# Kernel tuning notes

Hardware: AMD Instinct MI355X
Metric: run time of the kernel (lower is better)

The kernel has to match this reference:

```python
import jax, jax.numpy as jnp
import numpy as np

B, TQ, TK = 2, 2048, 2048
H, E, D = 16, 256, 4096       # num_heads, embed_dim, d_model
DH = D // H                   # head_dim == embed_dim (required by per-head RMSNorm(embed_dim))
LAMBDA_INIT = 0.8
LAYER_INDEX = 0
EPS = 1.1920929e-07           # torch RMSNorm default eps = finfo(float32).eps


def setup_inputs() -> dict:
    key = jax.random.key(0)
    ks = jax.random.split(key, 14)
    s = 0.02
    lam_init_val = LAMBDA_INIT - 0.6 * float(np.exp(-0.3 * LAYER_INDEX))
    return {
        "x": jax.random.normal(ks[0], (B, TQ, E), jnp.float32),
        "encoder_out": jax.random.normal(ks[1], (B, TK, E), jnp.float32),
        "Wq": jax.random.normal(ks[2], (H, E, DH), jnp.float32) * s,
        "bq": jnp.zeros((H, DH), jnp.float32),
        "Wk": jax.random.normal(ks[3], (H, E, DH), jnp.float32) * s,
        "bk": jnp.zeros((H, DH), jnp.float32),
        "Wv": jax.random.normal(ks[4], (H, E, DH), jnp.float32) * s,
        "bv": jnp.zeros((H, DH), jnp.float32),
        "lq1": jax.random.normal(ks[5], (H, DH), jnp.float32) * 0.1,
        "lk1": jax.random.normal(ks[6], (H, DH), jnp.float32) * 0.1,
        "lq2": jax.random.normal(ks[7], (H, DH), jnp.float32) * 0.1,
        "lk2": jax.random.normal(ks[8], (H, DH), jnp.float32) * 0.1,
        "lam_init": jnp.full((H,), lam_init_val, jnp.float32),
        "g": jnp.ones((H, DH), jnp.float32),     # per-head RMSNorm weight
        "Wo": jax.random.normal(ks[9], (D, E), jnp.float32) * s,
        "bo": jnp.zeros((E,), jnp.float32),
    }


def reference(x, encoder_out, Wq, bq, Wk, bk, Wv, bv,
              lq1, lk1, lq2, lk2, lam_init, g, Wo, bo):
    # per-head projections, vectorized over heads: [B,H,T,DH]
    q = jnp.einsum('bte,hed->bhtd', x, Wq) + bq[:, None, :]
    k = jnp.einsum('bse,hed->bhsd', encoder_out, Wk) + bk[:, None, :]
    v = jnp.einsum('bse,hed->bhsd', encoder_out, Wv) + bv[:, None, :]
    dh2 = DH // 2
    q1, q2 = q[..., :dh2], q[..., dh2:]
    k1, k2 = k[..., :dh2], k[..., dh2:]
    scale = 1.0 / jnp.sqrt(jnp.float32(dh2))
    s1 = jax.nn.softmax(jnp.einsum('bhtd,bhsd->bhts', q1, k1) * scale, axis=-1)
    s2 = jax.nn.softmax(jnp.einsum('bhtd,bhsd->bhts', q2, k2) * scale, axis=-1)
    # learned per-head lambda scalar
    lam = jnp.exp(jnp.sum(lq1 * lk1, axis=-1)) - jnp.exp(jnp.sum(lq2 * lk2, axis=-1)) + lam_init  # [H]
    w = s1 - lam[None, :, None, None] * s2
    o = jnp.einsum('bhts,bhsd->bhtd', w, v)
    # per-head RMSNorm + (1 - lambda_init) scaling
    rms = jnp.sqrt(jnp.mean(o * o, axis=-1, keepdims=True) + EPS)
    o = (1.0 - LAMBDA_INIT) * (o / rms) * g[None, :, None, :]
    # concat heads -> output projection
    o = o.transpose(0, 2, 1, 3).reshape(B, TQ, D)
    return o @ Wo + bo
```

## Files before the change

### kernel.cpp

```cpp
#include <hip/hip_runtime.h>
#include <hip/hip_bf16.h>
#include <stdint.h>
#include <math.h>

typedef __bf16 bf16;
typedef __bf16 bf16x8 __attribute__((ext_vector_type(8)));
typedef float f32x4 __attribute__((ext_vector_type(4)));
typedef unsigned int u32;

#define MFMA16(a, b, c) __builtin_amdgcn_mfma_f32_16x16x32_bf16(a, b, c, 0, 0, 0)

typedef const u32 __attribute__((address_space(1)))* gptr1;
typedef u32 __attribute__((address_space(3)))* lptr3;

__device__ __forceinline__ void load_lds16(const void* g, void* l) {
    __builtin_amdgcn_global_load_lds((gptr1)g, (lptr3)l, 16, 0, 0);
}

#define SCALE_QK 0.08838834764831845f
#define LOG2E 1.4426950408889634f
#define QK_PRESCALE (SCALE_QK * LOG2E)
#define RMS_EPS 1.1920929e-07f
#define OUT_SCALE 0.2f
#define DEFER_THR 8.0f

__global__ void cvt_act(const float* __restrict__ x, const float* __restrict__ enc,
                        bf16* __restrict__ xb, bf16* __restrict__ eb) {
    int gid = blockIdx.x * 256 + threadIdx.x;
    const float* src = (gid < 131072) ? x : enc;
    bf16* dst = (gid < 131072) ? xb : eb;
    int i = (gid & 131071) * 8;
    float4 v0 = *(const float4*)(src + i);
    float4 v1 = *(const float4*)(src + i + 4);
    union { bf16 h[8]; uint4 u; } p;
    p.h[0] = (bf16)v0.x; p.h[1] = (bf16)v0.y; p.h[2] = (bf16)v0.z; p.h[3] = (bf16)v0.w;
    p.h[4] = (bf16)v1.x; p.h[5] = (bf16)v1.y; p.h[6] = (bf16)v1.z; p.h[7] = (bf16)v1.w;
    *(uint4*)(dst + i) = p.u;
}

__global__ void txp_w(const float* __restrict__ Wq, const float* __restrict__ Wk,
                      const float* __restrict__ Wv,
                      bf16* __restrict__ WTq, bf16* __restrict__ WTk, bf16* __restrict__ WTv) {
    int z = blockIdx.z; int iw = z >> 4, hh = z & 15;
    const float* src = (iw == 0 ? Wq : iw == 1 ? Wk : Wv) + hh * 65536;
    bf16* dst = (iw == 0 ? WTq : iw == 1 ? WTk : WTv) + hh * 65536;
    __shared__ bf16 T[64][68];
    int r0 = blockIdx.y * 64, c0 = blockIdx.x * 64;
    int tid = threadIdx.x;
#pragma unroll
    for (int t = 0; t < 4; ++t) {
        int idx = tid + t * 256;
        int row = idx >> 4, c4 = (idx & 15) * 4;
        float4 v = *(const float4*)(src + (r0 + row) * 256 + c0 + c4);
        T[row][c4] = (bf16)v.x; T[row][c4 + 1] = (bf16)v.y;
        T[row][c4 + 2] = (bf16)v.z; T[row][c4 + 3] = (bf16)v.w;
    }
    __syncthreads();
#pragma unroll
    for (int t = 0; t < 2; ++t) {
        int idx = tid + t * 256;
        int crow = idx >> 3, r8 = (idx & 7) * 8;
        union { bf16 h[8]; uint4 u; } p;
#pragma unroll
        for (int j = 0; j < 8; ++j) p.h[j] = T[r8 + j][crow];
        *(uint4*)(dst + (c0 + crow) * 256 + r0 + r8) = p.u;
    }
}

__global__ void txp_wo(const float* __restrict__ Wo, bf16* __restrict__ WoT) {
    __shared__ bf16 T[64][68];
    int r0 = blockIdx.y * 64, c0 = blockIdx.x * 64;
    int tid = threadIdx.x;
#pragma unroll
    for (int t = 0; t < 4; ++t) {
        int idx = tid + t * 256;
        int row = idx >> 4, c4 = (idx & 15) * 4;
        float4 v = *(const float4*)(Wo + (size_t)(r0 + row) * 256 + c0 + c4);
        T[row][c4] = (bf16)v.x; T[row][c4 + 1] = (bf16)v.y;
        T[row][c4 + 2] = (bf16)v.z; T[row][c4 + 3] = (bf16)v.w;
    }
    __syncthreads();
#pragma unroll
    for (int t = 0; t < 2; ++t) {
        int idx = tid + t * 256;
        int crow = idx >> 3, r8 = (idx & 7) * 8;
        union { bf16 h[8]; uint4 u; } p;
#pragma unroll
        for (int j = 0; j < 8; ++j) p.h[j] = T[r8 + j][crow];
        *(uint4*)(WoT + (size_t)(c0 + crow) * 4096 + r0 + r8) = p.u;
    }
}

__global__ void txp_v(const bf16* __restrict__ V, bf16* __restrict__ VT) {
    int bh = blockIdx.z;
    const bf16* src = V + (size_t)bh * 2048 * 256;
    bf16* dst = VT + (size_t)bh * 256 * 2048;
    __shared__ bf16 T[64][68];
    int s0 = blockIdx.x * 64, d0 = blockIdx.y * 64;
    int tid = threadIdx.x;
#pragma unroll
    for (int t = 0; t < 2; ++t) {
        int idx = tid + t * 256;
        int row = idx >> 3, c8 = (idx & 7) * 8;
        uint4 v = *(const uint4*)(src + (s0 + row) * 256 + d0 + c8);
        *(uint2*)&T[row][c8] = make_uint2(v.x, v.y);
        *(uint2*)&T[row][c8 + 4] = make_uint2(v.z, v.w);
    }
    __syncthreads();
#pragma unroll
    for (int t = 0; t < 2; ++t) {
        int idx = tid + t * 256;
        int crow = idx >> 3, r8 = (idx & 7) * 8;
        union { bf16 h[8]; uint4 u; } p;
#pragma unroll
        for (int j = 0; j < 8; ++j) p.h[j] = T[r8 + j][crow];
        *(uint4*)(dst + (d0 + crow) * 2048 + s0 + r8) = p.u;
    }
}

__global__ void lam_kernel(const float* __restrict__ lq1, const float* __restrict__ lk1,
                           const float* __restrict__ lq2, const float* __restrict__ lk2,
                           const float* __restrict__ lam_init, float* __restrict__ lam_out) {
    int tid = threadIdx.x; int hh = tid >> 4, i = tid & 15;
    float s1 = 0.f, s2 = 0.f;
#pragma unroll
    for (int j = 0; j < 16; ++j) {
        int d = i + j * 16;
        s1 += lq1[hh * 256 + d] * lk1[hh * 256 + d];
        s2 += lq2[hh * 256 + d] * lk2[hh * 256 + d];
    }
#pragma unroll
    for (int msk = 1; msk < 16; msk <<= 1) { s1 += __shfl_xor(s1, msk); s2 += __shfl_xor(s2, msk); }
    if (i == 0) lam_out[hh] = __expf(s1) - __expf(s2) + lam_init[hh];
}

__global__ __launch_bounds__(256) void proj_gemm(
    const bf16* __restrict__ xb, const bf16* __restrict__ eb,
    const bf16* __restrict__ WTq, const bf16* __restrict__ WTk, const bf16* __restrict__ WTv,
    const float* __restrict__ bq, const float* __restrict__ bk, const float* __restrict__ bv,
    bf16* __restrict__ Qb, bf16* __restrict__ Kb, bf16* __restrict__ Vb) {
    int z = blockIdx.z;
    const bf16* A = (z == 0) ? xb : eb;
    const bf16* BT = (z == 0) ? WTq : (z == 1) ? WTk : WTv;
    const float* bias = (z == 0) ? bq : (z == 1) ? bk : bv;
    bf16* out = (z == 0) ? Qb : (z == 1) ? Kb : Vb;
    float qs = (z == 0) ? QK_PRESCALE : 1.0f;

    __shared__ alignas(16) bf16 As[128 * 32];
    __shared__ alignas(16) bf16 Bs[128 * 32];
    int m0 = blockIdx.x * 128, n0 = blockIdx.y * 128;
    int tid = threadIdx.x, w = tid >> 6, lane = tid & 63;
    int lrow = lane & 15, lgrp = lane >> 4, lk8 = lgrp * 8;
    int wr = (w >> 1) * 64, wc = (w & 1) * 64;

    f32x4 acc[4][4];
#pragma unroll
    for (int i = 0; i < 4; ++i)
#pragma unroll
        for (int j = 0; j < 4; ++j) acc[i][j] = (f32x4){0.f, 0.f, 0.f, 0.f};

    for (int k0 = 0; k0 < 256; k0 += 32) {
        __syncthreads();
#pragma unroll
        for (int t = 0; t < 2; ++t) {
            int c = tid + t * 256;
            int row = c >> 2, k8 = (c & 3) * 8;
            load_lds16(A + (m0 + row) * 256 + k0 + k8, &As[c * 8]);
            load_lds16(BT + (n0 + row) * 256 + k0 + k8, &Bs[c * 8]);
        }
        __syncthreads();
        bf16x8 af[4], bfr[4];
#pragma unroll
        for (int f = 0; f < 4; ++f) af[f] = *(const bf16x8*)&As[(wr + f * 16 + lrow) * 32 + lk8];
#pragma unroll
        for (int f = 0; f < 4; ++f) bfr[f] = *(const bf16x8*)&Bs[(wc + f * 16 + lrow) * 32 + lk8];
#pragma unroll
        for (int i = 0; i < 4; ++i)
#pragma unroll
            for (int j = 0; j < 4; ++j) acc[i][j] = MFMA16(af[i], bfr[j], acc[i][j]);
    }
#pragma unroll
    for (int i = 0; i < 4; ++i) {
#pragma unroll
        for (int j = 0; j < 4; ++j) {
            int n = n0 + wc + j * 16 + lrow;
            float bvv = bias[n];
            int hh = n >> 8, d = n & 255;
#pragma unroll
            for (int r = 0; r < 4; ++r) {
                int m = m0 + wr + i * 16 + lgrp * 4 + r;
                int bb = m >> 11, tt = m & 2047;
                out[(((size_t)bb * 16 + hh) * 2048 + tt) * 256 + d] = (bf16)((acc[i][j][r] + bvv) * qs);
            }
        }
    }
}

__global__ __launch_bounds__(256, 2) void attn_kernel(
    const bf16* __restrict__ Qb, const bf16* __restrict__ Kb, const bf16* __restrict__ VTb,
    const float* __restrict__ lam_ws, const float* __restrict__ g, bf16* __restrict__ On) {
    __shared__ alignas(16) bf16 Ks[2][32 * 256];
    __shared__ alignas(16) bf16 VTs[2][256 * 32];
    __shared__ alignas(16) bf16 Ps[4][16 * 72];

    int orig = blockIdx.x;
    int xcd = orig & 7, idx = orig >> 3;
    int bh = xcd * 4 + (idx >> 5);
    int qb = idx & 31;
    int b = bh >> 4, h = bh & 15;
    int q0 = qb * 64;

    int tid = threadIdx.x, w = tid >> 6, lane = tid & 63;
    int lrow = lane & 15, lgrp = lane >> 4, lk8 = lgrp * 8;
    int ksw = lrow & 7;
    int vsw = (lrow >> 1) & 3;

    const bf16* Qg = Qb + ((size_t)bh * 2048 + q0 + w * 16) * 256;
    bf16x8 qf[8];
#pragma unroll
    for (int kk = 0; kk < 8; ++kk)
        qf[kk] = *(const bf16x8*)(Qg + lrow * 256 + kk * 32 + lk8);

    f32x4 o1[16], o2[16];
#pragma unroll
    for (int i = 0; i < 16; ++i) { o1[i] = (f32x4){0.f,0.f,0.f,0.f}; o2[i] = (f32x4){0.f,0.f,0.f,0.f}; }
    float m1[4], l1[4], m2[4], l2[4];
#pragma unroll
    for (int r = 0; r < 4; ++r) { m1[r] = -1e30f; l1[r] = 0.f; m2[r] = -1e30f; l2[r] = 0.f; }

    const bf16* Kg = Kb + (size_t)bh * 2048 * 256;
    const bf16* VTg = VTb + (size_t)bh * 256 * 2048;
    bf16* Pw = &Ps[w][0];

    auto STAGE = [&](int buf, int kt) {
        int s0 = kt * 32;
#pragma unroll
        for (int i = 0; i < 4; ++i) {
            int s = i * 256 + tid;
            int row = s >> 5;
            int cg = (s & 31) ^ (row & 7);
            load_lds16(Kg + (size_t)(s0 + row) * 256 + cg * 8, &Ks[buf][s * 8]);
        }
#pragma unroll
        for (int i = 0; i < 4; ++i) {
            int s = i * 256 + tid;
            int row = s >> 2;
            int cg = (s & 3) ^ ((row >> 1) & 3);
            load_lds16(VTg + (size_t)row * 2048 + s0 + cg * 8, &VTs[buf][s * 8]);
        }
    };

    STAGE(0, 0);
    __syncthreads();

    int cur = 0;
    for (int kt = 0; kt < 64; ++kt) {
        if (kt + 1 < 64) STAGE(cur ^ 1, kt + 1);

        const bf16* Kbuf = &Ks[cur][0];
        const bf16* Vbuf = &VTs[cur][0];

        f32x4 s1a = (f32x4){0.f,0.f,0.f,0.f}, s1b = s1a, s2a = s1a, s2b = s1a;
        __builtin_amdgcn_s_setprio(1);
#pragma unroll
        for (int kk = 0; kk < 4; ++kk) {
            int c1 = (kk * 4 + lgrp) ^ ksw;
            int c2 = (16 + kk * 4 + lgrp) ^ ksw;
            bf16x8 k1a = *(const bf16x8*)&Kbuf[lrow * 256 + (c1 << 3)];
            bf16x8 k1b = *(const bf16x8*)&Kbuf[(16 + lrow) * 256 + (c1 << 3)];
            bf16x8 k2a = *(const bf16x8*)&Kbuf[lrow * 256 + (c2 << 3)];
            bf16x8 k2b = *(const bf16x8*)&Kbuf[(16 + lrow) * 256 + (c2 << 3)];
            s1a = MFMA16(qf[kk], k1a, s1a);
            s1b = MFMA16(qf[kk], k1b, s1b);
            s2a = MFMA16(qf[4 + kk], k2a, s2a);
            s2b = MFMA16(qf[4 + kk], k2b, s2b);
        }
        __builtin_amdgcn_s_setprio(0);

        float lmx1 = fmaxf(fmaxf(s1a[0], s1b[0]), fmaxf(s1a[1], s1b[1]));
        lmx1 = fmaxf(lmx1, fmaxf(fmaxf(s1a[2], s1b[2]), fmaxf(s1a[3], s1b[3])));
        float lmx2 = fmaxf(fmaxf(s2a[0], s2b[0]), fmaxf(s2a[1], s2b[1]));
        lmx2 = fmaxf(lmx2, fmaxf(fmaxf(s2a[2], s2b[2]), fmaxf(s2a[3], s2b[3])));
        float mmin1 = fminf(fminf(m1[0], m1[1]), fminf(m1[2], m1[3]));
        float mmin2 = fminf(fminf(m2[0], m2[1]), fminf(m2[2], m2[3]));

        if (!__all((lmx1 <= mmin1 + DEFER_THR) ? 1 : 0)) {
            float mt[4];
#pragma unroll
            for (int r = 0; r < 4; ++r) mt[r] = fmaxf(s1a[r], s1b[r]);
#pragma unroll
            for (int msk = 1; msk < 16; msk <<= 1)
#pragma unroll
                for (int r = 0; r < 4; ++r) mt[r] = fmaxf(mt[r], __shfl_xor(mt[r], msk));
            float c[4];
#pragma unroll
            for (int r = 0; r < 4; ++r) {
                float mn = fmaxf(m1[r], mt[r]);
                c[r] = exp2f(m1[r] - mn);
                m1[r] = mn; l1[r] *= c[r];
            }
#pragma unroll
            for (int df = 0; df < 16; ++df)
#pragma unroll
                for (int r = 0; r < 4; ++r) o1[df][r] *= c[r];
        }
        if (!__all((lmx2 <= mmin2 + DEFER_THR) ? 1 : 0)) {
            float mt[4];
#pragma unroll
            for (int r = 0; r < 4; ++r) mt[r] = fmaxf(s2a[r], s2b[r]);
#pragma unroll
            for (int msk = 1; msk < 16; msk <<= 1)
#pragma unroll
                for (int r = 0; r < 4; ++r) mt[r] = fmaxf(mt[r], __shfl_xor(mt[r], msk));
            float c[4];
#pragma unroll
            for (int r = 0; r < 4; ++r) {
                float mn = fmaxf(m2[r], mt[r]);
                c[r] = exp2f(m2[r] - mn);
                m2[r] = mn; l2[r] *= c[r];
            }
#pragma unroll
            for (int df = 0; df < 16; ++df)
#pragma unroll
                for (int r = 0; r < 4; ++r) o2[df][r] *= c[r];
        }
#pragma unroll
        for (int r = 0; r < 4; ++r) {
            float p10 = exp2f(s1a[r] - m1[r]);
            float p11 = exp2f(s1b[r] - m1[r]);
            float p20 = exp2f(s2a[r] - m2[r]);
            float p21 = exp2f(s2b[r] - m2[r]);
            l1[r] += p10 + p11;
            l2[r] += p20 + p21;
            int prow = (lgrp * 4 + r) * 72;
            Pw[prow + lrow] = (bf16)p10;
            Pw[prow + 16 + lrow] = (bf16)p11;
            Pw[prow + 32 + lrow] = (bf16)p20;
            Pw[prow + 48 + lrow] = (bf16)p21;
        }

        bf16x8 pa1 = *(const bf16x8*)&Pw[lrow * 72 + lk8];
        bf16x8 pa2 = *(const bf16x8*)&Pw[lrow * 72 + 32 + lk8];
        __builtin_amdgcn_s_setprio(1);
#pragma unroll
        for (int df = 0; df < 16; ++df) {
            int vc = lgrp ^ vsw;
            bf16x8 vb = *(const bf16x8*)&Vbuf[(df * 16 + lrow) * 32 + (vc << 3)];
            o1[df] = MFMA16(pa1, vb, o1[df]);
            o2[df] = MFMA16(pa2, vb, o2[df]);
        }
        __builtin_amdgcn_s_setprio(0);

        __syncthreads();
        cur ^= 1;
    }

#pragma unroll
    for (int msk = 1; msk < 16; msk <<= 1)
#pragma unroll
        for (int r = 0; r < 4; ++r) {
            l1[r] += __shfl_xor(l1[r], msk);
            l2[r] += __shfl_xor(l2[r], msk);
        }
    float lam = lam_ws[h];
    float i1[4], i2[4], ssq[4];
#pragma unroll
    for (int r = 0; r < 4; ++r) { i1[r] = 1.f / l1[r]; i2[r] = lam / l2[r]; ssq[r] = 0.f; }
#pragma unroll
    for (int df = 0; df < 16; ++df)
#pragma unroll
        for (int r = 0; r < 4; ++r) {
            float v = o1[df][r] * i1[r] - o2[df][r] * i2[r];
            o1[df][r] = v;
            ssq[r] += v * v;
        }
#pragma unroll
    for (int msk = 1; msk < 16; msk <<= 1)
#pragma unroll
        for (int r = 0; r < 4; ++r) ssq[r] += __shfl_xor(ssq[r], msk);
    float rinv[4];
#pragma unroll
    for (int r = 0; r < 4; ++r) rinv[r] = 1.f / sqrtf(ssq[r] * (1.f / 256.f) + RMS_EPS);
#pragma unroll
    for (int df = 0; df < 16; ++df) {
        int d = df * 16 + lrow;
        float gv = g[h * 256 + d] * OUT_SCALE;
#pragma unroll
        for (int r = 0; r < 4; ++r) {
            int t = q0 + w * 16 + lgrp * 4 + r;
            On[((size_t)b * 2048 + t) * 4096 + h * 256 + d] = (bf16)(o1[df][r] * rinv[r] * gv);
        }
    }
}

__global__ __launch_bounds__(256) void out_gemm(const bf16* __restrict__ A, const bf16* __restrict__ BT,
                                                const float* __restrict__ bo, float* __restrict__ out) {
    __shared__ alignas(16) bf16 As[64 * 32];
    __shared__ alignas(16) bf16 Bs[64 * 32];
    int m0 = blockIdx.x * 64, n0 = blockIdx.y * 64;
    int tid = threadIdx.x, w = tid >> 6, lane = tid & 63;
    int lrow = lane & 15, lgrp = lane >> 4, lk8 = lgrp * 8;
    int wr = (w >> 1) * 32, wc = (w & 1) * 32;
    f32x4 acc[2][2];
#pragma unroll
    for (int i = 0; i < 2; ++i)
#pragma unroll
        for (int j = 0; j < 2; ++j) acc[i][j] = (f32x4){0.f, 0.f, 0.f, 0.f};
    for (int k0 = 0; k0 < 4096; k0 += 32) {
        __syncthreads();
        int row = tid >> 2, k8 = (tid & 3) * 8;
        load_lds16(A + (size_t)(m0 + row) * 4096 + k0 + k8, &As[tid * 8]);
        load_lds16(BT + (size_t)(n0 + row) * 4096 + k0 + k8, &Bs[tid * 8]);
        __syncthreads();
        bf16x8 af[2], bfr[2];
#pragma unroll
        for (int f = 0; f < 2; ++f) {
            af[f] = *(const bf16x8*)&As[(wr + f * 16 + lrow) * 32 + lk8];
            bfr[f] = *(const bf16x8*)&Bs[(wc + f * 16 + lrow) * 32 + lk8];
        }
#pragma unroll
        for (int i = 0; i < 2; ++i)
#pragma unroll
            for (int j = 0; j < 2; ++j) acc[i][j] = MFMA16(af[i], bfr[j], acc[i][j]);
    }
#pragma unroll
    for (int i = 0; i < 2; ++i)
#pragma unroll
        for (int j = 0; j < 2; ++j) {
            int n = n0 + wc + j * 16 + lrow;
            float bv = bo[n];
#pragma unroll
            for (int r = 0; r < 4; ++r) {
                int m = m0 + wr + i * 16 + lgrp * 4 + r;
                out[(size_t)m * 256 + n] = acc[i][j][r] + bv;
            }
        }
}

extern "C" void kernel_launch(void* const* d_in, const int* in_sizes, int n_in,
                              void* d_out, int out_size, void* d_ws, size_t ws_size,
                              hipStream_t stream) {
    const float* x = (const float*)d_in[0];
    const float* enc = (const float*)d_in[1];
    const float* Wq = (const float*)d_in[2];
    const float* bq = (const float*)d_in[3];
    const float* Wk = (const float*)d_in[4];
    const float* bk = (const float*)d_in[5];
    const float* Wv = (const float*)d_in[6];
    const float* bv = (const float*)d_in[7];
    const float* lq1 = (const float*)d_in[8];
    const float* lk1 = (const float*)d_in[9];
    const float* lq2 = (const float*)d_in[10];
    const float* lk2 = (const float*)d_in[11];
    const float* lam_init = (const float*)d_in[12];
    const float* g = (const float*)d_in[13];
    const float* Wo = (const float*)d_in[14];
    const float* bo = (const float*)d_in[15];
    float* out = (float*)d_out;

    char* ws = (char*)d_ws;
    const size_t MB = 1024 * 1024;
    bf16* xb  = (bf16*)(ws + 0 * MB);
    bf16* eb  = (bf16*)(ws + 2 * MB);
    bf16* WTq = (bf16*)(ws + 4 * MB);
    bf16* WTk = (bf16*)(ws + 6 * MB);
    bf16* WTv = (bf16*)(ws + 8 * MB);
    bf16* WoT = (bf16*)(ws + 10 * MB);
    float* lam = (float*)(ws + 12 * MB);
    bf16* Qb  = (bf16*)(ws + 13 * MB);
    bf16* Kb  = (bf16*)(ws + 45 * MB);
    bf16* Vb  = (bf16*)(ws + 77 * MB);
    bf16* VTb = (bf16*)(ws + 109 * MB);
    bf16* On  = Vb;

    hipLaunchKernelGGL(cvt_act, dim3(1024), dim3(256), 0, stream, x, enc, xb, eb);
    hipLaunchKernelGGL(txp_w, dim3(4, 4, 48), dim3(256), 0, stream, Wq, Wk, Wv, WTq, WTk, WTv);
    hipLaunchKernelGGL(txp_wo, dim3(4, 64, 1), dim3(256), 0, stream, Wo, WoT);
    hipLaunchKernelGGL(lam_kernel, dim3(1), dim3(256), 0, stream, lq1, lk1, lq2, lk2, lam_init, lam);
    hipLaunchKernelGGL(proj_gemm, dim3(32, 32, 3), dim3(256), 0, stream,
                       xb, eb, WTq, WTk, WTv, bq, bk, bv, Qb, Kb, Vb);
    hipLaunchKernelGGL(txp_v, dim3(32, 4, 32), dim3(256), 0, stream, Vb, VTb);
    hipLaunchKernelGGL(attn_kernel, dim3(1024), dim3(256), 0, stream, Qb, Kb, VTb, lam, g, On);
    hipLaunchKernelGGL(out_gemm, dim3(64, 4), dim3(256), 0, stream, On, WoT, bo, out);
}
```

Baseline: 385.8 us.

## Switch attention to 32x32 MFMA with per-wave softmax branch split

Rewrites the attention kernel so each wave owns one of the two differential softmax branches for 32 query rows and uses 32x32x16 MFMA. The score tile is computed transposed (K as A operand), and probabilities are repacked into the PV operand with cross-half lane shuffles instead of a round trip through shared memory. Per-row rescale factors are exchanged through LDS, and the two branches are combined at the end through a shared-memory buffer before the RMSNorm. The aim is higher MFMA efficiency, fewer LDS P writes and fewer registers per wave. The cost is extra LDS traffic and barriers in the epilogue, plus a larger shared-memory footprint that may limit occupancy.

```diff
diff --git a/kernel.cpp b/kernel.cpp
--- a/kernel.cpp
+++ b/kernel.cpp
@@ -6,15 +6,26 @@
 typedef __bf16 bf16;
 typedef __bf16 bf16x8 __attribute__((ext_vector_type(8)));
 typedef float f32x4 __attribute__((ext_vector_type(4)));
+typedef float f32x16 __attribute__((ext_vector_type(16)));
 typedef unsigned int u32;
 
 #define MFMA16(a, b, c) __builtin_amdgcn_mfma_f32_16x16x32_bf16(a, b, c, 0, 0, 0)
+#define MFMA32(a, b, c) __builtin_amdgcn_mfma_f32_32x32x16_bf16(a, b, c, 0, 0, 0)
 
 typedef const u32 __attribute__((address_space(1)))* gptr1;
 typedef u32 __attribute__((address_space(3)))* lptr3;
 
 __device__ __forceinline__ void load_lds16(const void* g, void* l) {
     __builtin_amdgcn_global_load_lds((gptr1)g, (lptr3)l, 16, 0, 0);
+}
+
+__device__ __forceinline__ u32 pk2(float lo, float hi_) {
+    union { bf16 h[2]; u32 u; } t;
+    t.h[0] = (bf16)lo; t.h[1] = (bf16)hi_;
+    return t.u;
+}
+__device__ __forceinline__ u32 xswap(u32 x) {
+    return (u32)__shfl_xor((int)x, 32);
 }
 
 #define SCALE_QK 0.08838834764831845f
@@ -199,9 +210,14 @@
 __global__ __launch_bounds__(256, 2) void attn_kernel(
     const bf16* __restrict__ Qb, const bf16* __restrict__ Kb, const bf16* __restrict__ VTb,
     const float* __restrict__ lam_ws, const float* __restrict__ g, bf16* __restrict__ On) {
-    __shared__ alignas(16) bf16 Ks[2][32 * 256];
-    __shared__ alignas(16) bf16 VTs[2][256 * 32];
-    __shared__ alignas(16) bf16 Ps[4][16 * 72];
+    __shared__ alignas(16) char SMEM[75264];
+    bf16* KsB = (bf16*)SMEM;
+    bf16* VsB = (bf16*)(SMEM + 32768);
+    float* o2buf  = (float*)SMEM;
+    float* smem_c = (float*)(SMEM + 65536);
+    float* smem_i = (float*)(SMEM + 66048);
+    float* smem_r = (float*)(SMEM + 66560);
+    float* psum   = (float*)(SMEM + 66816);
 
     int orig = blockIdx.x;
     int xcd = orig & 7, idx = orig >> 3;
@@ -211,26 +227,27 @@
     int q0 = qb * 64;
 
     int tid = threadIdx.x, w = tid >> 6, lane = tid & 63;
-    int lrow = lane & 15, lgrp = lane >> 4, lk8 = lgrp * 8;
-    int ksw = lrow & 7;
-    int vsw = (lrow >> 1) & 3;
-
-    const bf16* Qg = Qb + ((size_t)bh * 2048 + q0 + w * 16) * 256;
+    int lq = lane & 31, hi = lane >> 5;
+    int br = w >> 1, qw = (w & 1) * 32;
+    int ksw = lq & 7;
+    int vsw = (lq >> 1) & 3;
+    bool hib = (hi != 0);
+
+    const bf16* Qg = Qb + ((size_t)bh * 2048 + q0 + qw + lq) * 256 + br * 128;
     bf16x8 qf[8];
 #pragma unroll
-    for (int kk = 0; kk < 8; ++kk)
-        qf[kk] = *(const bf16x8*)(Qg + lrow * 256 + kk * 32 + lk8);
-
-    f32x4 o1[16], o2[16];
-#pragma unroll
-    for (int i = 0; i < 16; ++i) { o1[i] = (f32x4){0.f,0.f,0.f,0.f}; o2[i] = (f32x4){0.f,0.f,0.f,0.f}; }
-    float m1[4], l1[4], m2[4], l2[4];
-#pragma unroll
-    for (int r = 0; r < 4; ++r) { m1[r] = -1e30f; l1[r] = 0.f; m2[r] = -1e30f; l2[r] = 0.f; }
+    for (int dk = 0; dk < 8; ++dk)
+        qf[dk] = *(const bf16x8*)(Qg + dk * 16 + hi * 8);
+
+    f32x16 o[8];
+#pragma unroll
+    for (int dt = 0; dt < 8; ++dt)
+#pragma unroll
+        for (int i = 0; i < 16; ++i) o[dt][i] = 0.f;
+    float m = -1e30f, lsum = 0.f;
 
     const bf16* Kg = Kb + (size_t)bh * 2048 * 256;
     const bf16* VTg = VTb + (size_t)bh * 256 * 2048;
-    bf16* Pw = &Ps[w][0];
 
     auto STAGE = [&](int buf, int kt) {
         int s0 = kt * 32;
@@ -239,14 +256,14 @@
             int s = i * 256 + tid;
             int row = s >> 5;
             int cg = (s & 31) ^ (row & 7);
-            load_lds16(Kg + (size_t)(s0 + row) * 256 + cg * 8, &Ks[buf][s * 8]);
+            load_lds16(Kg + (size_t)(s0 + row) * 256 + cg * 8, KsB + buf * 8192 + s * 8);
         }
 #pragma unroll
         for (int i = 0; i < 4; ++i) {
             int s = i * 256 + tid;
             int row = s >> 2;
             int cg = (s & 3) ^ ((row >> 1) & 3);
-            load_lds16(VTg + (size_t)row * 2048 + s0 + cg * 8, &VTs[buf][s * 8]);
+            load_lds16(VTg + (size_t)row * 2048 + s0 + cg * 8, VsB + buf * 8192 + s * 8);
         }
     };
 
@@ -256,98 +273,77 @@
     int cur = 0;
     for (int kt = 0; kt < 64; ++kt) {
         if (kt + 1 < 64) STAGE(cur ^ 1, kt + 1);
-
-        const bf16* Kbuf = &Ks[cur][0];
-        const bf16* Vbuf = &VTs[cur][0];
-
-        f32x4 s1a = (f32x4){0.f,0.f,0.f,0.f}, s1b = s1a, s2a = s1a, s2b = s1a;
+        const bf16* Kbuf = KsB + cur * 8192;
+        const bf16* Vbuf = VsB + cur * 8192;
+
+        f32x16 sa, sb;
+#pragma unroll
+        for (int i = 0; i < 16; ++i) { sa[i] = 0.f; sb[i] = 0.f; }
         __builtin_amdgcn_s_setprio(1);
 #pragma unroll
-        for (int kk = 0; kk < 4; ++kk) {
-            int c1 = (kk * 4 + lgrp) ^ ksw;
-            int c2 = (16 + kk * 4 + lgrp) ^ ksw;
-            bf16x8 k1a = *(const bf16x8*)&Kbuf[lrow * 256 + (c1 << 3)];
-            bf16x8 k1b = *(const bf16x8*)&Kbuf[(16 + lrow) * 256 + (c1 << 3)];
-            bf16x8 k2a = *(const bf16x8*)&Kbuf[lrow * 256 + (c2 << 3)];
-            bf16x8 k2b = *(const bf16x8*)&Kbuf[(16 + lrow) * 256 + (c2 << 3)];
-            s1a = MFMA16(qf[kk], k1a, s1a);
-            s1b = MFMA16(qf[kk], k1b, s1b);
-            s2a = MFMA16(qf[4 + kk], k2a, s2a);
-            s2b = MFMA16(qf[4 + kk], k2b, s2b);
+        for (int dk = 0; dk < 4; ++dk) {
+            bf16x8 k0 = *(const bf16x8*)&Kbuf[lq * 256 + (((br * 16 + 4 * dk + hi) ^ ksw) << 3)];
+            bf16x8 k1 = *(const bf16x8*)&Kbuf[lq * 256 + (((br * 16 + 4 * dk + 2 + hi) ^ ksw) << 3)];
+            sa = MFMA32(k0, qf[2 * dk], sa);
+            sb = MFMA32(k1, qf[2 * dk + 1], sb);
         }
         __builtin_amdgcn_s_setprio(0);
-
-        float lmx1 = fmaxf(fmaxf(s1a[0], s1b[0]), fmaxf(s1a[1], s1b[1]));
-        lmx1 = fmaxf(lmx1, fmaxf(fmaxf(s1a[2], s1b[2]), fmaxf(s1a[3], s1b[3])));
-        float lmx2 = fmaxf(fmaxf(s2a[0], s2b[0]), fmaxf(s2a[1], s2b[1]));
-        lmx2 = fmaxf(lmx2, fmaxf(fmaxf(s2a[2], s2b[2]), fmaxf(s2a[3], s2b[3])));
-        float mmin1 = fminf(fminf(m1[0], m1[1]), fminf(m1[2], m1[3]));
-        float mmin2 = fminf(fminf(m2[0], m2[1]), fminf(m2[2], m2[3]));
-
-        if (!__all((lmx1 <= mmin1 + DEFER_THR) ? 1 : 0)) {
-            float mt[4];
-#pragma unroll
-            for (int r = 0; r < 4; ++r) mt[r] = fmaxf(s1a[r], s1b[r]);
-#pragma unroll
-            for (int msk = 1; msk < 16; msk <<= 1)
-#pragma unroll
-                for (int r = 0; r < 4; ++r) mt[r] = fmaxf(mt[r], __shfl_xor(mt[r], msk));
-            float c[4];
-#pragma unroll
-            for (int r = 0; r < 4; ++r) {
-                float mn = fmaxf(m1[r], mt[r]);
-                c[r] = exp2f(m1[r] - mn);
-                m1[r] = mn; l1[r] *= c[r];
+        f32x16 sc;
+#pragma unroll
+        for (int i = 0; i < 16; ++i) sc[i] = sa[i] + sb[i];
+
+        float m0a = fmaxf(sc[0], sc[1]),  m0b = fmaxf(sc[2], sc[3]);
+        float m0c = fmaxf(sc[4], sc[5]),  m0d = fmaxf(sc[6], sc[7]);
+        float m0e = fmaxf(sc[8], sc[9]),  m0f = fmaxf(sc[10], sc[11]);
+        float m0g = fmaxf(sc[12], sc[13]), m0h = fmaxf(sc[14], sc[15]);
+        float mt = fmaxf(fmaxf(fmaxf(m0a, m0b), fmaxf(m0c, m0d)),
+                         fmaxf(fmaxf(m0e, m0f), fmaxf(m0g, m0h)));
+        mt = fmaxf(mt, __shfl_xor(mt, 32));
+
+        if (!__all((mt <= m + DEFER_THR) ? 1 : 0)) {
+            float mn = fmaxf(m, mt);
+            float corr = exp2f(m - mn);
+            smem_c[w * 32 + lq] = corr;
+            asm volatile("s_waitcnt lgkmcnt(0)" ::: "memory");
+            m = mn; lsum *= corr;
+#pragma unroll
+            for (int r = 0; r < 16; ++r) {
+                float cg = smem_c[w * 32 + (r & 3) + 8 * (r >> 2) + 4 * hi];
+#pragma unroll
+                for (int dt = 0; dt < 8; ++dt) o[dt][r] *= cg;
             }
-#pragma unroll
-            for (int df = 0; df < 16; ++df)
-#pragma unroll
-                for (int r = 0; r < 4; ++r) o1[df][r] *= c[r];
-        }
-        if (!__all((lmx2 <= mmin2 + DEFER_THR) ? 1 : 0)) {
-            float mt[4];
-#pragma unroll
-            for (int r = 0; r < 4; ++r) mt[r] = fmaxf(s2a[r], s2b[r]);
-#pragma unroll
-            for (int msk = 1; msk < 16; msk <<= 1)
-#pragma unroll
-                for (int r = 0; r < 4; ++r) mt[r] = fmaxf(mt[r], __shfl_xor(mt[r], msk));
-            float c[4];
-#pragma unroll
-            for (int r = 0; r < 4; ++r) {
-                float mn = fmaxf(m2[r], mt[r]);
-                c[r] = exp2f(m2[r] - mn);
-                m2[r] = mn; l2[r] *= c[r];
-            }
-#pragma unroll
-            for (int df = 0; df < 16; ++df)
-#pragma unroll
-                for (int r = 0; r < 4; ++r) o2[df][r] *= c[r];
-        }
-#pragma unroll
-        for (int r = 0; r < 4; ++r) {
-            float p10 = exp2f(s1a[r] - m1[r]);
-            float p11 = exp2f(s1b[r] - m1[r]);
-            float p20 = exp2f(s2a[r] - m2[r]);
-            float p21 = exp2f(s2b[r] - m2[r]);
-            l1[r] += p10 + p11;
-            l2[r] += p20 + p21;
-            int prow = (lgrp * 4 + r) * 72;
-            Pw[prow + lrow] = (bf16)p10;
-            Pw[prow + 16 + lrow] = (bf16)p11;
-            Pw[prow + 32 + lrow] = (bf16)p20;
-            Pw[prow + 48 + lrow] = (bf16)p21;
-        }
-
-        bf16x8 pa1 = *(const bf16x8*)&Pw[lrow * 72 + lk8];
-        bf16x8 pa2 = *(const bf16x8*)&Pw[lrow * 72 + 32 + lk8];
+        }
+
+        float p[16];
+        float ls0 = 0.f, ls1 = 0.f;
+#pragma unroll
+        for (int i = 0; i < 8; ++i) { p[i] = exp2f(sc[i] - m); ls0 += p[i]; }
+#pragma unroll
+        for (int i = 8; i < 16; ++i) { p[i] = exp2f(sc[i] - m); ls1 += p[i]; }
+        lsum += ls0 + ls1;
+
+        u32 X0 = pk2(p[0], p[1]),   X1 = pk2(p[2], p[3]);
+        u32 Y0 = pk2(p[4], p[5]),   Y1 = pk2(p[6], p[7]);
+        u32 Z0 = pk2(p[8], p[9]),   Z1 = pk2(p[10], p[11]);
+        u32 W0 = pk2(p[12], p[13]), W1 = pk2(p[14], p[15]);
+        u32 pX0 = xswap(X0), pX1 = xswap(X1);
+        u32 pY0 = xswap(Y0), pY1 = xswap(Y1);
+        u32 pZ0 = xswap(Z0), pZ1 = xswap(Z1);
+        u32 pW0 = xswap(W0), pW1 = xswap(W1);
+        union { u32 u[4]; bf16x8 v; } PA0, PA1;
+        PA0.u[0] = hib ? pY0 : X0;  PA0.u[1] = hib ? pY1 : X1;
+        PA0.u[2] = hib ? Y0 : pX0;  PA0.u[3] = hib ? Y1 : pX1;
+        PA1.u[0] = hib ? pW0 : Z0;  PA1.u[1] = hib ? pW1 : Z1;
+        PA1.u[2] = hib ? W0 : pZ0;  PA1.u[3] = hib ? W1 : pZ1;
+
         __builtin_amdgcn_s_setprio(1);
 #pragma unroll
-        for (int df = 0; df < 16; ++df) {
-            int vc = lgrp ^ vsw;
-            bf16x8 vb = *(const bf16x8*)&Vbuf[(df * 16 + lrow) * 32 + (vc << 3)];
-            o1[df] = MFMA16(pa1, vb, o1[df]);
-            o2[df] = MFMA16(pa2, vb, o2[df]);
+        for (int dt = 0; dt < 8; ++dt) {
+            const bf16* vrow = &Vbuf[(dt * 32 + lq) * 32];
+            bf16x8 v0 = *(const bf16x8*)&vrow[(hi ^ vsw) << 3];
+            o[dt] = MFMA32(PA0.v, v0, o[dt]);
+            bf16x8 v1 = *(const bf16x8*)&vrow[((2 + hi) ^ vsw) << 3];
+            o[dt] = MFMA32(PA1.v, v1, o[dt]);
         }
         __builtin_amdgcn_s_setprio(0);
 
@@ -355,40 +351,61 @@
         cur ^= 1;
     }
 
-#pragma unroll
-    for (int msk = 1; msk < 16; msk <<= 1)
-#pragma unroll
-        for (int r = 0; r < 4; ++r) {
-            l1[r] += __shfl_xor(l1[r], msk);
-            l2[r] += __shfl_xor(l2[r], msk);
-        }
+    lsum += __shfl_xor(lsum, 32);
     float lam = lam_ws[h];
-    float i1[4], i2[4], ssq[4];
-#pragma unroll
-    for (int r = 0; r < 4; ++r) { i1[r] = 1.f / l1[r]; i2[r] = lam / l2[r]; ssq[r] = 0.f; }
-#pragma unroll
-    for (int df = 0; df < 16; ++df)
-#pragma unroll
-        for (int r = 0; r < 4; ++r) {
-            float v = o1[df][r] * i1[r] - o2[df][r] * i2[r];
-            o1[df][r] = v;
-            ssq[r] += v * v;
-        }
-#pragma unroll
-    for (int msk = 1; msk < 16; msk <<= 1)
-#pragma unroll
-        for (int r = 0; r < 4; ++r) ssq[r] += __shfl_xor(ssq[r], msk);
-    float rinv[4];
-#pragma unroll
-    for (int r = 0; r < 4; ++r) rinv[r] = 1.f / sqrtf(ssq[r] * (1.f / 256.f) + RMS_EPS);
-#pragma unroll
-    for (int df = 0; df < 16; ++df) {
-        int d = df * 16 + lrow;
-        float gv = g[h * 256 + d] * OUT_SCALE;
-#pragma unroll
-        for (int r = 0; r < 4; ++r) {
-            int t = q0 + w * 16 + lgrp * 4 + r;
-            On[((size_t)b * 2048 + t) * 4096 + h * 256 + d] = (bf16)(o1[df][r] * rinv[r] * gv);
+    float inv = (br == 0) ? 1.f / lsum : lam / lsum;
+    smem_i[br * 64 + qw + lq] = inv;
+    __syncthreads();
+
+    if (br == 1) {
+#pragma unroll
+        for (int r = 0; r < 16; ++r) {
+            int qp = (r & 3) + 8 * (r >> 2) + 4 * hi + qw;
+            float i2 = smem_i[64 + qp];
+#pragma unroll
+            for (int dt = 0; dt < 8; ++dt)
+                o2buf[qp * 256 + dt * 32 + lq] = o[dt][r] * i2;
+        }
+    }
+    __syncthreads();
+
+    if (br == 0) {
+#pragma unroll
+        for (int r = 0; r < 16; ++r) {
+            int qp = (r & 3) + 8 * (r >> 2) + 4 * hi + qw;
+            float i1 = smem_i[qp];
+            float ss = 0.f;
+#pragma unroll
+            for (int dt = 0; dt < 8; ++dt) {
+                float v = o[dt][r] * i1 - o2buf[qp * 256 + dt * 32 + lq];
+                o[dt][r] = v;
+                ss += v * v;
+            }
+            psum[qp * 33 + lq] = ss;
+        }
+    }
+    __syncthreads();
+
+    if (tid < 64) {
+        float s = 0.f;
+#pragma unroll
+        for (int i = 0; i < 32; ++i) s += psum[tid * 33 + i];
+        smem_r[tid] = 1.f / sqrtf(s * (1.f / 256.f) + RMS_EPS);
+    }
+    __syncthreads();
+
+    if (br == 0) {
+        float gv[8];
+#pragma unroll
+        for (int dt = 0; dt < 8; ++dt) gv[dt] = g[h * 256 + dt * 32 + lq] * OUT_SCALE;
+#pragma unroll
+        for (int r = 0; r < 16; ++r) {
+            int qp = (r & 3) + 8 * (r >> 2) + 4 * hi + qw;
+            float rv = smem_r[qp];
+            size_t base = ((size_t)b * 2048 + q0 + qp) * 4096 + h * 256;
+#pragma unroll
+            for (int dt = 0; dt < 8; ++dt)
+                On[base + dt * 32 + lq] = (bf16)(o[dt][r] * rv * gv[dt]);
         }
     }
 }
```

Measured after the change: 375.9 us. 2.6% less time.
